# Kernel tuning notes

Measured on AMD Instinct MI355X. Metric: run time of the kernel, lower is better.

The kernel has to match this reference:

```python
import jax, jax.numpy as jnp
import numpy as np

N = 100000      # nodes
E = 1600000     # edges (before self-loops)
F_IN = 128      # num_features
C = 32          # embedding_dim / output_dim per head
H = 4           # heads
SLOPE = 0.2     # PyG GATv2Conv default negative_slope


def setup_inputs() -> dict:
    key = jax.random.key(0)
    ks = jax.random.split(key, 16)
    def w(k, shp, fan):
        return jax.random.normal(k, shp, jnp.float32) / np.float32(np.sqrt(fan))
    return {
        "x": jax.random.normal(ks[0], (N, F_IN), jnp.float32),
        "edge_index": jax.random.randint(ks[1], (2, E), 0, N, jnp.int32),
        "W1l": w(ks[2], (F_IN, H * C), F_IN),
        "W1r": w(ks[3], (F_IN, H * C), F_IN),
        "att1": w(ks[4], (H, C), C),
        "b1": jnp.zeros((H * C,), jnp.float32),
        "W2l": w(ks[5], (H * C, H * C), H * C),
        "W2r": w(ks[6], (H * C, H * C), H * C),
        "att2": w(ks[7], (H, C), C),
        "b2": jnp.zeros((H * C,), jnp.float32),
        "W3l": w(ks[8], (H * C, H * C), H * C),
        "W3r": w(ks[9], (H * C, H * C), H * C),
        "att3": w(ks[10], (H, C), C),
        "b3": jnp.zeros((C,), jnp.float32),
    }


def gatv2_conv(x, src, dst, Wl, Wr, att, b, concat):
    """GATv2Conv: gather -> LeakyReLU attention -> segment softmax -> scatter-add."""
    n = x.shape[0]
    h, c = att.shape
    xl = (x @ Wl).reshape(n, h, c)   # source-side projection
    xr = (x @ Wr).reshape(n, h, c)   # target-side projection
    e = jax.nn.leaky_relu(xl[src] + xr[dst], SLOPE)          # [E, H, C]
    logits = jnp.einsum('ehc,hc->eh', e, att)                # [E, H]
    m = jax.ops.segment_max(logits, dst, num_segments=n)     # per-dst max
    ex = jnp.exp(logits - m[dst])
    den = jax.ops.segment_sum(ex, dst, num_segments=n)
    alpha = ex / den[dst]                                    # [E, H]
    out = jax.ops.segment_sum(alpha[:, :, None] * xl[src], dst, num_segments=n)  # [N,H,C]
    out = out.reshape(n, h * c) if concat else out.mean(axis=1)
    return out + b


def reference(x, edge_index, W1l, W1r, att1, b1, W2l, W2r, att2, b2, W3l, W3r, att3, b3):
    n = x.shape[0]
    loops = jnp.arange(n, dtype=edge_index.dtype)            # PyG adds self-loops
    src = jnp.concatenate([edge_index[0], loops])
    dst = jnp.concatenate([edge_index[1], loops])
    h = jax.nn.relu(gatv2_conv(x, src, dst, W1l, W1r, att1, b1, True))
    h = jax.nn.relu(gatv2_conv(h, src, dst, W2l, W2r, att2, b2, True))
    h = jax.nn.relu(gatv2_conv(h, src, dst, W3l, W3r, att3, b3, False))
    return h
```

## Files before the change

### kernel.cpp

```cpp
#include <hip/hip_runtime.h>
#include <hip/hip_bf16.h>
#include <hip/hip_fp16.h>

#define SLOPE 0.2f

typedef __attribute__((ext_vector_type(8))) short bf16x8;
typedef __attribute__((ext_vector_type(4))) float f32x4;

__device__ __forceinline__ unsigned short bf16_rn(float f) {
    unsigned u = __float_as_uint(f);
    return (unsigned short)((u + 0x7FFFu + ((u >> 16) & 1u)) >> 16);
}
__device__ __forceinline__ float bf16_to_f32(unsigned short s) {
    return __uint_as_float(((unsigned)s) << 16);
}


__global__ __launch_bounds__(256) void k_init(int* deg, int* cnt, int n) {
    int i = blockIdx.x * 256 + threadIdx.x;
    if (i < n) { deg[i] = 1; cnt[i] = 0; }
}

__global__ __launch_bounds__(256) void k_hist(const int* __restrict__ dstv, int* deg, int E) {
    int i = blockIdx.x * 256 + threadIdx.x;
    if (i < E) atomicAdd(&deg[dstv[i]], 1);
}

__global__ __launch_bounds__(256) void k_scan(const int* __restrict__ in, int* __restrict__ out,
                                              int* bsums, int n) {
    __shared__ int wsum[4];
    int t = threadIdx.x;
    int base = blockIdx.x * 1024 + t * 4;
    int v0 = (base + 0 < n) ? in[base + 0] : 0;
    int v1 = (base + 1 < n) ? in[base + 1] : 0;
    int v2 = (base + 2 < n) ? in[base + 2] : 0;
    int v3 = (base + 3 < n) ? in[base + 3] : 0;
    int tsum = v0 + v1 + v2 + v3;
    int lane = t & 63, wid = t >> 6;
    int x = tsum;
    #pragma unroll
    for (int d = 1; d < 64; d <<= 1) {
        int y = __shfl_up(x, d);
        if (lane >= d) x += y;
    }
    if (lane == 63) wsum[wid] = x;
    __syncthreads();
    if (t == 0) {
        int a = 0;
        for (int w = 0; w < 4; ++w) { int b = wsum[w]; wsum[w] = a; a += b; }
    }
    __syncthreads();
    int excl = x - tsum + wsum[wid];
    if (base + 0 < n) out[base + 0] = excl;
    if (base + 1 < n) out[base + 1] = excl + v0;
    if (base + 2 < n) out[base + 2] = excl + v0 + v1;
    if (base + 3 < n) out[base + 3] = excl + v0 + v1 + v2;
    if (bsums != nullptr && t == 255) bsums[blockIdx.x] = excl + tsum;
}

__global__ __launch_bounds__(256) void k_scan_add(const int* __restrict__ dscan,
                                                  const int* __restrict__ boff,
                                                  int* __restrict__ rowptr, int n, int total) {
    int i = blockIdx.x * 256 + threadIdx.x;
    if (i < n) rowptr[i] = dscan[i] + boff[i >> 10];
    if (i == n) rowptr[n] = total;
}

__global__ __launch_bounds__(256) void k_fill(const int* __restrict__ srcv, const int* __restrict__ dstv,
                                              const int* __restrict__ rowptr, int* cnt, int* col,
                                              int E, int n) {
    int i = blockIdx.x * 256 + threadIdx.x;
    if (i < E) {
        int d = dstv[i];
        int pos = rowptr[d] + atomicAdd(&cnt[d], 1);
        col[pos] = srcv[i];
    } else if (i < E + n) {
        int d = i - E;
        int pos = rowptr[d] + atomicAdd(&cnt[d], 1);
        col[pos] = d;
    }
}


__global__ __launch_bounds__(256) void k_wprep(const float* __restrict__ W,
                                               unsigned short* __restrict__ hiT,
                                               unsigned short* __restrict__ loT) {
    int e = blockIdx.x * 256 + threadIdx.x;
    int n = e >> 7, k = e & 127;
    float x = W[k * 128 + n];
    unsigned short h = bf16_rn(x);
    hiT[e] = h;
    loT[e] = bf16_rn(x - bf16_to_f32(h));
}


#define LDS_A_HI 0
#define LDS_A_LO 10240
#define LDS_B_HI 20480
#define LDS_B_LO 30720

__global__ __launch_bounds__(256) void k_gemm(const float* __restrict__ X,
                                              const unsigned short* __restrict__ Whi,
                                              const unsigned short* __restrict__ Wlo,
                                              __half* __restrict__ Y0, float* __restrict__ Y1,
                                              int M) {
    __shared__ __align__(16) unsigned char lds[40960];
    const unsigned short* whi = Whi + (size_t)blockIdx.y * 16384;
    const unsigned short* wlo = Wlo + (size_t)blockIdx.y * 16384;
    int t = threadIdx.x;
    int row0 = blockIdx.x * 128;
    int lane = t & 63, w = t >> 6;
    int ml = lane & 15, q = lane >> 4;

    int sm = t >> 1;
    int sh = t & 1;
    int srow = row0 + sm;
    bool svalid = srow < M;

    f32x4 acc[2][8];
    #pragma unroll
    for (int i = 0; i < 2; ++i)
        #pragma unroll
        for (int j = 0; j < 8; ++j) acc[i][j] = (f32x4){0.f, 0.f, 0.f, 0.f};

    for (int ks = 0; ks < 4; ++ks) {
        int k0 = ks * 32;
        {
            float v[16];
            if (svalid) {
                const float* src = X + (size_t)srow * 128 + k0 + sh * 16;
                *(float4*)&v[0]  = *(const float4*)&src[0];
                *(float4*)&v[4]  = *(const float4*)&src[4];
                *(float4*)&v[8]  = *(const float4*)&src[8];
                *(float4*)&v[12] = *(const float4*)&src[12];
            } else {
                #pragma unroll
                for (int j = 0; j < 16; ++j) v[j] = 0.f;
            }
            unsigned hw[8], lw[8];
            #pragma unroll
            for (int j = 0; j < 8; ++j) {
                unsigned short h0 = bf16_rn(v[2 * j]);
                unsigned short h1 = bf16_rn(v[2 * j + 1]);
                unsigned short l0 = bf16_rn(v[2 * j] - bf16_to_f32(h0));
                unsigned short l1 = bf16_rn(v[2 * j + 1] - bf16_to_f32(h1));
                hw[j] = (unsigned)h0 | ((unsigned)h1 << 16);
                lw[j] = (unsigned)l0 | ((unsigned)l1 << 16);
            }
            unsigned char* pa = lds + LDS_A_HI + sm * 80 + sh * 32;
            *(uint4*)(pa)      = *(uint4*)&hw[0];
            *(uint4*)(pa + 16) = *(uint4*)&hw[4];
            unsigned char* pl = lds + LDS_A_LO + sm * 80 + sh * 32;
            *(uint4*)(pl)      = *(uint4*)&lw[0];
            *(uint4*)(pl + 16) = *(uint4*)&lw[4];
        }
        {
            #pragma unroll
            for (int cc = 0; cc < 2; ++cc) {
                int c = t + cc * 256;
                int n = c >> 2, kc = (c & 3) * 8;
                *(uint4*)(lds + LDS_B_HI + n * 80 + (c & 3) * 16) =
                    *(const uint4*)(whi + n * 128 + k0 + kc);
                *(uint4*)(lds + LDS_B_LO + n * 80 + (c & 3) * 16) =
                    *(const uint4*)(wlo + n * 128 + k0 + kc);
            }
        }
        __syncthreads();
        bf16x8 ah[2], al[2];
        #pragma unroll
        for (int mt = 0; mt < 2; ++mt) {
            int am = w * 32 + mt * 16 + ml;
            ah[mt] = *(const bf16x8*)(lds + LDS_A_HI + am * 80 + q * 16);
            al[mt] = *(const bf16x8*)(lds + LDS_A_LO + am * 80 + q * 16);
        }
        #pragma unroll
        for (int nt = 0; nt < 8; ++nt) {
            int bn = nt * 16 + ml;
            bf16x8 bh = *(const bf16x8*)(lds + LDS_B_HI + bn * 80 + q * 16);
            bf16x8 bl = *(const bf16x8*)(lds + LDS_B_LO + bn * 80 + q * 16);
            #pragma unroll
            for (int mt = 0; mt < 2; ++mt) {
                acc[mt][nt] = __builtin_amdgcn_mfma_f32_16x16x32_bf16(ah[mt], bh, acc[mt][nt], 0, 0, 0);
                acc[mt][nt] = __builtin_amdgcn_mfma_f32_16x16x32_bf16(ah[mt], bl, acc[mt][nt], 0, 0, 0);
                acc[mt][nt] = __builtin_amdgcn_mfma_f32_16x16x32_bf16(al[mt], bh, acc[mt][nt], 0, 0, 0);
            }
        }
        __syncthreads();
    }

    if (blockIdx.y == 0) {
        #pragma unroll
        for (int mt = 0; mt < 2; ++mt) {
            int rbase = row0 + w * 32 + mt * 16 + q * 4;
            #pragma unroll
            for (int r = 0; r < 4; ++r) {
                int row = rbase + r;
                if (row < M) {
                    #pragma unroll
                    for (int nt = 0; nt < 8; ++nt)
                        Y0[(size_t)row * 128 + nt * 16 + ml] = __float2half(acc[mt][nt][r]);
                }
            }
        }
    } else {
        #pragma unroll
        for (int mt = 0; mt < 2; ++mt) {
            int rbase = row0 + w * 32 + mt * 16 + q * 4;
            #pragma unroll
            for (int r = 0; r < 4; ++r) {
                int row = rbase + r;
                if (row < M) {
                    #pragma unroll
                    for (int nt = 0; nt < 8; ++nt)
                        Y1[(size_t)row * 128 + nt * 16 + ml] = acc[mt][nt][r];
                }
            }
        }
    }
}


__device__ __forceinline__ float quadsum(float t) {
    t += __int_as_float(__builtin_amdgcn_update_dpp(0, __float_as_int(t), 0xB1, 0xf, 0xf, true));
    t += __int_as_float(__builtin_amdgcn_update_dpp(0, __float_as_int(t), 0x4E, 0xf, 0xf, true));
    return t;
}

template <bool MEAN>
__global__ __launch_bounds__(256) void fused_gat(const __half* __restrict__ XLh,
                                                 const float* __restrict__ XR,
                                                 const float* __restrict__ att,
                                                 const float* __restrict__ bias,
                                                 const int* __restrict__ rowptr,
                                                 const int* __restrict__ col,
                                                 float* __restrict__ OUT, int N) {
    int wave = (blockIdx.x * blockDim.x + threadIdx.x) >> 6;
    int lane = threadIdx.x & 63;
    int g = lane >> 4, sub = lane & 15;
    int dst = wave * 4 + g;
    bool vd = dst < N;

    int start = vd ? rowptr[dst] : 0;
    int end   = vd ? rowptr[dst + 1] : 0;

    float xr[8], av[8];
    {
        const float* xrp = &XR[(size_t)(vd ? dst : 0) * 128 + sub * 8];
        *(float4*)&xr[0] = *(const float4*)&xrp[0];
        *(float4*)&xr[4] = *(const float4*)&xrp[4];
        *(float4*)&av[0] = *(const float4*)&att[sub * 8];
        *(float4*)&av[4] = *(const float4*)&att[sub * 8 + 4];
    }

    int deg = end - start;
    int md = max(deg, __shfl_xor(deg, 16));
    md = max(md, __shfl_xor(md, 32));

    float acc[8];
    #pragma unroll
    for (int j = 0; j < 8; ++j) acc[j] = 0.f;
    float s = 0.f;

    for (int i = 0; i < md; i += 2) {
        int pA = start + i, pB = start + i + 1;
        bool vA = pA < end, vB = pB < end;
        int iA = col[vA ? pA : 0];
        int iB = col[vB ? pB : 0];
        uint4 rA = *(const uint4*)&XLh[(size_t)iA * 128 + sub * 8];
        uint4 rB = *(const uint4*)&XLh[(size_t)iB * 128 + sub * 8];
        float xA[8], xB[8];
        {
            const __half2* hA = (const __half2*)&rA;
            const __half2* hB = (const __half2*)&rB;
            #pragma unroll
            for (int qq = 0; qq < 4; ++qq) {
                float2 fA = __half22float2(hA[qq]);
                float2 fB = __half22float2(hB[qq]);
                xA[2 * qq] = fA.x; xA[2 * qq + 1] = fA.y;
                xB[2 * qq] = fB.x; xB[2 * qq + 1] = fB.y;
            }
        }
        float dA = 0.f, dB = 0.f;
        #pragma unroll
        for (int j = 0; j < 8; ++j) {
            float uA = xA[j] + xr[j];
            float uB = xB[j] + xr[j];
            uA = fmaxf(uA, SLOPE * uA);
            uB = fmaxf(uB, SLOPE * uB);
            dA = fmaf(uA, av[j], dA);
            dB = fmaf(uB, av[j], dB);
        }
        float tA = quadsum(dA);
        float tB = quadsum(dB);
        float wA = __expf(fminf(tA, 80.f));
        float wB = __expf(fminf(tB, 80.f));
        wA = vA ? wA : 0.f;
        wB = vB ? wB : 0.f;
        s += wA + wB;
        #pragma unroll
        for (int j = 0; j < 8; ++j) {
            acc[j] = fmaf(wA, xA[j], acc[j]);
            acc[j] = fmaf(wB, xB[j], acc[j]);
        }
    }

    float rs = 1.0f / s;
    if (MEAN) {
        float o[8];
        #pragma unroll
        for (int j = 0; j < 8; ++j) {
            float v = acc[j] * rs;
            v += __shfl_xor(v, 4);
            v += __shfl_xor(v, 8);
            o[j] = fmaxf(fmaf(v, 0.25f, bias[sub * 8 + j]), 0.f);
        }
        if (vd && sub < 4) {
            *(float4*)&OUT[(size_t)dst * 32 + sub * 8]     = *(float4*)&o[0];
            *(float4*)&OUT[(size_t)dst * 32 + sub * 8 + 4] = *(float4*)&o[4];
        }
    } else {
        float o[8];
        #pragma unroll
        for (int j = 0; j < 8; ++j)
            o[j] = fmaxf(fmaf(acc[j], rs, bias[sub * 8 + j]), 0.f);
        if (vd) {
            *(float4*)&OUT[(size_t)dst * 128 + sub * 8]     = *(float4*)&o[0];
            *(float4*)&OUT[(size_t)dst * 128 + sub * 8 + 4] = *(float4*)&o[4];
        }
    }
}


extern "C" void kernel_launch(void* const* d_in, const int* in_sizes, int n_in,
                              void* d_out, int out_size, void* d_ws, size_t ws_size,
                              hipStream_t stream) {
    const float* x   = (const float*)d_in[0];
    const int*   ei  = (const int*)d_in[1];
    const float* W1l = (const float*)d_in[2];
    const float* W1r = (const float*)d_in[3];
    const float* at1 = (const float*)d_in[4];
    const float* b1  = (const float*)d_in[5];
    const float* W2l = (const float*)d_in[6];
    const float* W2r = (const float*)d_in[7];
    const float* at2 = (const float*)d_in[8];
    const float* b2  = (const float*)d_in[9];
    const float* W3l = (const float*)d_in[10];
    const float* W3r = (const float*)d_in[11];
    const float* at3 = (const float*)d_in[12];
    const float* b3  = (const float*)d_in[13];
    float* out = (float*)d_out;

    int N = in_sizes[0] / 128;
    int E = in_sizes[1] / 2;
    int ET = E + N;
    const int* srcv = ei;
    const int* dstv = ei + E;

    char* p = (char*)d_ws;
    auto alloc = [&](size_t bytes) -> void* {
        void* r = (void*)p;
        p += (bytes + 255) & ~(size_t)255;
        return r;
    };
    __half* XLh = (__half*)alloc((size_t)N * 128 * 2);
    float*  XR  = (float*)alloc((size_t)N * 128 * 4);
    float*  H   = (float*)alloc((size_t)N * 128 * 4);
    int* rowptr = (int*)alloc((size_t)(N + 1) * 4);
    int* deg    = (int*)alloc((size_t)N * 4);
    int* dscan  = (int*)alloc((size_t)N * 4);
    int* cnt    = (int*)alloc((size_t)N * 4);
    int* bsum   = (int*)alloc(1024 * 4);
    int* boff   = (int*)alloc(1024 * 4);
    int* col    = (int*)alloc((size_t)ET * 4);
    unsigned short* Wtab = (unsigned short*)alloc((size_t)6 * 65536 * 2);

    const float* Ws[6] = { W1l, W1r, W2l, W2r, W3l, W3r };
    for (int j = 0; j < 6; ++j) {
        int L = j >> 1, side = j & 1;
        unsigned short* hiT = Wtab + (size_t)L * 65536 + side * 16384;
        unsigned short* loT = hiT + 32768;
        k_wprep<<<64, 256, 0, stream>>>(Ws[j], hiT, loT);
    }

    k_init<<<(N + 255) / 256, 256, 0, stream>>>(deg, cnt, N);
    k_hist<<<(E + 255) / 256, 256, 0, stream>>>(dstv, deg, E);
    int nb = (N + 1023) / 1024;
    k_scan<<<nb, 256, 0, stream>>>(deg, dscan, bsum, N);
    k_scan<<<1, 256, 0, stream>>>(bsum, boff, nullptr, nb);
    k_scan_add<<<(N + 256) / 256, 256, 0, stream>>>(dscan, boff, rowptr, N, ET);
    k_fill<<<(ET + 255) / 256, 256, 0, stream>>>(srcv, dstv, rowptr, cnt, col, E, N);

    dim3 gg((N + 127) / 128, 2);
    int nfb = (N + 15) / 16;

    k_gemm<<<gg, 256, 0, stream>>>(x, Wtab + 0 * 65536, Wtab + 0 * 65536 + 32768, XLh, XR, N);
    fused_gat<false><<<nfb, 256, 0, stream>>>(XLh, XR, at1, b1, rowptr, col, H, N);
    k_gemm<<<gg, 256, 0, stream>>>(H, Wtab + 1 * 65536, Wtab + 1 * 65536 + 32768, XLh, XR, N);
    fused_gat<false><<<nfb, 256, 0, stream>>>(XLh, XR, at2, b2, rowptr, col, H, N);
    k_gemm<<<gg, 256, 0, stream>>>(H, Wtab + 2 * 65536, Wtab + 2 * 65536 + 32768, XLh, XR, N);
    fused_gat<true><<<nfb, 256, 0, stream>>>(XLh, XR, at3, b3, rowptr, col, out, N);
}
```

Baseline: 607.0 us.

## Fuse prep launches, overlap histogram with first GEMM, handle self-loops inline

Merges the six weight-prep launches and the degree init into one kernel. The first GEMM and the degree histogram now run in a single launch, with the histogram in extra blocks. Self-loops are no longer stored in the CSR; each destination's own term is computed directly in fused_gat before the neighbour loop. The fill kernel loads four edges at once through int4 reads and a cursor array. This cuts launch count, CSR build traffic and per-edge gather work, at the cost of more complex kernels and a heavier first launch.

```diff
diff --git a/kernel.cpp b/kernel.cpp
--- a/kernel.cpp
+++ b/kernel.cpp
@@ -16,15 +16,30 @@
 }
 
 
-__global__ __launch_bounds__(256) void k_init(int* deg, int* cnt, int n) {
-    int i = blockIdx.x * 256 + threadIdx.x;
-    if (i < n) { deg[i] = 1; cnt[i] = 0; }
-}
-
-__global__ __launch_bounds__(256) void k_hist(const int* __restrict__ dstv, int* deg, int E) {
-    int i = blockIdx.x * 256 + threadIdx.x;
-    if (i < E) atomicAdd(&deg[dstv[i]], 1);
-}
+__global__ __launch_bounds__(256) void fat_prep(const float* __restrict__ W0, const float* __restrict__ W1,
+                                                const float* __restrict__ W2, const float* __restrict__ W3,
+                                                const float* __restrict__ W4, const float* __restrict__ W5,
+                                                unsigned short* __restrict__ Wtab, int* __restrict__ deg, int N) {
+    int b = blockIdx.x, t = threadIdx.x;
+    if (b < 384) {
+        int j = b >> 6;
+        int e = ((b & 63) << 8) + t;
+        const float* W = (j == 0) ? W0 : (j == 1) ? W1 : (j == 2) ? W2
+                       : (j == 3) ? W3 : (j == 4) ? W4 : W5;
+        int L = j >> 1, side = j & 1;
+        unsigned short* hiT = Wtab + (size_t)L * 65536 + side * 16384;
+        unsigned short* loT = hiT + 32768;
+        int n = e >> 7, k = e & 127;
+        float x = W[k * 128 + n];
+        unsigned short h = bf16_rn(x);
+        hiT[e] = h;
+        loT[e] = bf16_rn(x - bf16_to_f32(h));
+    } else {
+        int i = (b - 384) * 256 + t;
+        if (i < N) deg[i] = 0;
+    }
+}
+
 
 __global__ __launch_bounds__(256) void k_scan(const int* __restrict__ in, int* __restrict__ out,
                                               int* bsums, int n) {
@@ -60,37 +75,41 @@
 
 __global__ __launch_bounds__(256) void k_scan_add(const int* __restrict__ dscan,
                                                   const int* __restrict__ boff,
-                                                  int* __restrict__ rowptr, int n, int total) {
+                                                  int* __restrict__ rowptr, int* __restrict__ cursor,
+                                                  int n, int total) {
     int i = blockIdx.x * 256 + threadIdx.x;
-    if (i < n) rowptr[i] = dscan[i] + boff[i >> 10];
+    if (i < n) {
+        int v = dscan[i] + boff[i >> 10];
+        rowptr[i] = v;
+        cursor[i] = v;
+    }
     if (i == n) rowptr[n] = total;
 }
 
+
 __global__ __launch_bounds__(256) void k_fill(const int* __restrict__ srcv, const int* __restrict__ dstv,
-                                              const int* __restrict__ rowptr, int* cnt, int* col,
-                                              int E, int n) {
-    int i = blockIdx.x * 256 + threadIdx.x;
-    if (i < E) {
-        int d = dstv[i];
-        int pos = rowptr[d] + atomicAdd(&cnt[d], 1);
-        col[pos] = srcv[i];
-    } else if (i < E + n) {
-        int d = i - E;
-        int pos = rowptr[d] + atomicAdd(&cnt[d], 1);
-        col[pos] = d;
-    }
-}
-
-
-__global__ __launch_bounds__(256) void k_wprep(const float* __restrict__ W,
-                                               unsigned short* __restrict__ hiT,
-                                               unsigned short* __restrict__ loT) {
-    int e = blockIdx.x * 256 + threadIdx.x;
-    int n = e >> 7, k = e & 127;
-    float x = W[k * 128 + n];
-    unsigned short h = bf16_rn(x);
-    hiT[e] = h;
-    loT[e] = bf16_rn(x - bf16_to_f32(h));
+                                              int* __restrict__ cursor, int* __restrict__ col, int E) {
+    int base = blockIdx.x * 1024 + threadIdx.x * 4;
+    if (base + 3 < E) {
+        int4 s4 = *(const int4*)&srcv[base];
+        int4 d4 = *(const int4*)&dstv[base];
+        int p0 = atomicAdd(&cursor[d4.x], 1);
+        int p1 = atomicAdd(&cursor[d4.y], 1);
+        int p2 = atomicAdd(&cursor[d4.z], 1);
+        int p3 = atomicAdd(&cursor[d4.w], 1);
+        col[p0] = s4.x;
+        col[p1] = s4.y;
+        col[p2] = s4.z;
+        col[p3] = s4.w;
+    } else {
+        for (int j = 0; j < 4; ++j) {
+            int i = base + j;
+            if (i < E) {
+                int p = atomicAdd(&cursor[dstv[i]], 1);
+                col[p] = srcv[i];
+            }
+        }
+    }
 }
 
 
@@ -99,21 +118,18 @@
 #define LDS_B_HI 20480
 #define LDS_B_LO 30720
 
-__global__ __launch_bounds__(256) void k_gemm(const float* __restrict__ X,
-                                              const unsigned short* __restrict__ Whi,
-                                              const unsigned short* __restrict__ Wlo,
-                                              __half* __restrict__ Y0, float* __restrict__ Y1,
-                                              int M) {
-    __shared__ __align__(16) unsigned char lds[40960];
-    const unsigned short* whi = Whi + (size_t)blockIdx.y * 16384;
-    const unsigned short* wlo = Wlo + (size_t)blockIdx.y * 16384;
-    int t = threadIdx.x;
-    int row0 = blockIdx.x * 128;
+__device__ __forceinline__ void gemm_block(const float* __restrict__ X,
+                                           const unsigned short* __restrict__ Whi,
+                                           const unsigned short* __restrict__ Wlo,
+                                           __half* __restrict__ Y0, float* __restrict__ Y1,
+                                           int M, int tile, int ysel,
+                                           unsigned char* lds, int t) {
+    const unsigned short* whi = Whi + (size_t)ysel * 16384;
+    const unsigned short* wlo = Wlo + (size_t)ysel * 16384;
+    int row0 = tile * 128;
     int lane = t & 63, w = t >> 6;
     int ml = lane & 15, q = lane >> 4;
-
-    int sm = t >> 1;
-    int sh = t & 1;
+    int sm = t >> 1, sh = t & 1;
     int srow = row0 + sm;
     bool svalid = srow < M;
 
@@ -188,7 +204,7 @@
         __syncthreads();
     }
 
-    if (blockIdx.y == 0) {
+    if (ysel == 0) {
         #pragma unroll
         for (int mt = 0; mt < 2; ++mt) {
             int rbase = row0 + w * 32 + mt * 16 + q * 4;
@@ -215,6 +231,40 @@
                         Y1[(size_t)row * 128 + nt * 16 + ml] = acc[mt][nt][r];
                 }
             }
+        }
+    }
+}
+
+__global__ __launch_bounds__(256) void k_gemm(const float* __restrict__ X,
+                                              const unsigned short* __restrict__ Whi,
+                                              const unsigned short* __restrict__ Wlo,
+                                              __half* __restrict__ Y0, float* __restrict__ Y1, int M) {
+    __shared__ __align__(16) unsigned char lds[40960];
+    gemm_block(X, Whi, Wlo, Y0, Y1, M, blockIdx.x, blockIdx.y, lds, threadIdx.x);
+}
+
+
+__global__ __launch_bounds__(256) void fat_hg(const float* __restrict__ X,
+                                              const unsigned short* __restrict__ Whi,
+                                              const unsigned short* __restrict__ Wlo,
+                                              __half* __restrict__ Y0, float* __restrict__ Y1, int M,
+                                              const int* __restrict__ dstv, int* __restrict__ deg, int E) {
+    __shared__ __align__(16) unsigned char lds[40960];
+    int tiles = (M + 127) >> 7;
+    int b = blockIdx.x;
+    if (b < 2 * tiles) {
+        gemm_block(X, Whi, Wlo, Y0, Y1, M, b % tiles, b / tiles, lds, threadIdx.x);
+    } else {
+        int base = (b - 2 * tiles) * 1024 + threadIdx.x * 4;
+        if (base + 3 < E) {
+            int4 d4 = *(const int4*)&dstv[base];
+            atomicAdd(&deg[d4.x], 1);
+            atomicAdd(&deg[d4.y], 1);
+            atomicAdd(&deg[d4.z], 1);
+            atomicAdd(&deg[d4.w], 1);
+        } else {
+            for (int j = 0; j < 4; ++j)
+                if (base + j < E) atomicAdd(&deg[dstv[base + j]], 1);
         }
     }
 }
@@ -239,13 +289,14 @@
     int g = lane >> 4, sub = lane & 15;
     int dst = wave * 4 + g;
     bool vd = dst < N;
-
-    int start = vd ? rowptr[dst] : 0;
-    int end   = vd ? rowptr[dst + 1] : 0;
+    int d0 = vd ? dst : 0;
+
+    int start = vd ? rowptr[d0] : 0;
+    int end   = vd ? rowptr[d0 + 1] : 0;
 
     float xr[8], av[8];
     {
-        const float* xrp = &XR[(size_t)(vd ? dst : 0) * 128 + sub * 8];
+        const float* xrp = &XR[(size_t)d0 * 128 + sub * 8];
         *(float4*)&xr[0] = *(const float4*)&xrp[0];
         *(float4*)&xr[4] = *(const float4*)&xrp[4];
         *(float4*)&av[0] = *(const float4*)&att[sub * 8];
@@ -257,9 +308,29 @@
     md = max(md, __shfl_xor(md, 32));
 
     float acc[8];
-    #pragma unroll
-    for (int j = 0; j < 8; ++j) acc[j] = 0.f;
-    float s = 0.f;
+    float s;
+    {
+        uint4 r = *(const uint4*)&XLh[(size_t)d0 * 128 + sub * 8];
+        float xs[8];
+        const __half2* h = (const __half2*)&r;
+        #pragma unroll
+        for (int qq = 0; qq < 4; ++qq) {
+            float2 f = __half22float2(h[qq]);
+            xs[2 * qq] = f.x; xs[2 * qq + 1] = f.y;
+        }
+        float dS = 0.f;
+        #pragma unroll
+        for (int j = 0; j < 8; ++j) {
+            float u = xs[j] + xr[j];
+            u = fmaxf(u, SLOPE * u);
+            dS = fmaf(u, av[j], dS);
+        }
+        float tS = quadsum(dS);
+        float wS = __expf(fminf(tS, 80.f));
+        s = wS;
+        #pragma unroll
+        for (int j = 0; j < 8; ++j) acc[j] = wS * xs[j];
+    }
 
     for (int i = 0; i < md; i += 2) {
         int pA = start + i, pB = start + i + 1;
@@ -352,7 +423,6 @@
 
     int N = in_sizes[0] / 128;
     int E = in_sizes[1] / 2;
-    int ET = E + N;
     const int* srcv = ei;
     const int* dstv = ei + E;
 
@@ -368,35 +438,27 @@
     int* rowptr = (int*)alloc((size_t)(N + 1) * 4);
     int* deg    = (int*)alloc((size_t)N * 4);
     int* dscan  = (int*)alloc((size_t)N * 4);
-    int* cnt    = (int*)alloc((size_t)N * 4);
+    int* cursor = (int*)alloc((size_t)N * 4);
     int* bsum   = (int*)alloc(1024 * 4);
     int* boff   = (int*)alloc(1024 * 4);
-    int* col    = (int*)alloc((size_t)ET * 4);
+    int* col    = (int*)alloc((size_t)E * 4);
     unsigned short* Wtab = (unsigned short*)alloc((size_t)6 * 65536 * 2);
 
-    const float* Ws[6] = { W1l, W1r, W2l, W2r, W3l, W3r };
-    for (int j = 0; j < 6; ++j) {
-        int L = j >> 1, side = j & 1;
-        unsigned short* hiT = Wtab + (size_t)L * 65536 + side * 16384;
-        unsigned short* loT = hiT + 32768;
-        k_wprep<<<64, 256, 0, stream>>>(Ws[j], hiT, loT);
-    }
-
-    k_init<<<(N + 255) / 256, 256, 0, stream>>>(deg, cnt, N);
-    k_hist<<<(E + 255) / 256, 256, 0, stream>>>(dstv, deg, E);
+    int tiles = (N + 127) / 128;
+    int nfb = (N + 15) / 16;
+    int hblocks = (E + 1023) / 1024;
+
+    fat_prep<<<384 + (N + 255) / 256, 256, 0, stream>>>(W1l, W1r, W2l, W2r, W3l, W3r, Wtab, deg, N);
+    fat_hg<<<2 * tiles + hblocks, 256, 0, stream>>>(x, Wtab, Wtab + 32768, XLh, XR, N, dstv, deg, E);
     int nb = (N + 1023) / 1024;
     k_scan<<<nb, 256, 0, stream>>>(deg, dscan, bsum, N);
     k_scan<<<1, 256, 0, stream>>>(bsum, boff, nullptr, nb);
-    k_scan_add<<<(N + 256) / 256, 256, 0, stream>>>(dscan, boff, rowptr, N, ET);
-    k_fill<<<(ET + 255) / 256, 256, 0, stream>>>(srcv, dstv, rowptr, cnt, col, E, N);
-
-    dim3 gg((N + 127) / 128, 2);
-    int nfb = (N + 15) / 16;
-
-    k_gemm<<<gg, 256, 0, stream>>>(x, Wtab + 0 * 65536, Wtab + 0 * 65536 + 32768, XLh, XR, N);
+    k_scan_add<<<(N + 256) / 256, 256, 0, stream>>>(dscan, boff, rowptr, cursor, N, E);
+    k_fill<<<hblocks, 256, 0, stream>>>(srcv, dstv, cursor, col, E);
+
     fused_gat<false><<<nfb, 256, 0, stream>>>(XLh, XR, at1, b1, rowptr, col, H, N);
-    k_gemm<<<gg, 256, 0, stream>>>(H, Wtab + 1 * 65536, Wtab + 1 * 65536 + 32768, XLh, XR, N);
+    k_gemm<<<dim3(tiles, 2), 256, 0, stream>>>(H, Wtab + 1 * 65536, Wtab + 1 * 65536 + 32768, XLh, XR, N);
     fused_gat<false><<<nfb, 256, 0, stream>>>(XLh, XR, at2, b2, rowptr, col, H, N);
-    k_gemm<<<gg, 256, 0, stream>>>(H, Wtab + 2 * 65536, Wtab + 2 * 65536 + 32768, XLh, XR, N);
+    k_gemm<<<dim3(tiles, 2), 256, 0, stream>>>(H, Wtab + 2 * 65536, Wtab + 2 * 65536 + 32768, XLh, XR, N);
     fused_gat<true><<<nfb, 256, 0, stream>>>(XLh, XR, at3, b3, rowptr, col, out, N);
 }
```

Measured after the change: 651.8 us. 7.4% more time.
